# Kernel tuning notes

Measured on AMD Instinct MI355X. Metric: run time of the kernel, lower is better.

Reference implementation:

```python
import jax, jax.numpy as jnp
import numpy as np
import math

DIM = 1024
NUM_HEADS = 16
HEAD_DIM = DIM // NUM_HEADS
WINDOW = 256


def setup_inputs() -> dict:
    key = jax.random.key(0)
    k1, k2, k3 = jax.random.split(key, 3)
    B, T = 2, 2048
    x = jax.random.normal(k1, (B, T, DIM), dtype=jnp.float32)
    # nn.Linear weights: [out, in]; y = x @ W.T
    w_qkv = jax.random.normal(k2, (3 * DIM, DIM), dtype=jnp.float32) * (1.0 / math.sqrt(DIM))
    w_out = jax.random.normal(k3, (DIM, DIM), dtype=jnp.float32) * (1.0 / math.sqrt(DIM))
    return {"x": x, "w_qkv": w_qkv, "w_out": w_out}


def _apply_rotary(x, cos, sin):
    # x: [B,H,T,D]; cos/sin: [T, D//2] broadcast over B,H
    d = x.shape[-1] // 2
    x1, x2 = x[..., :d], x[..., d:]
    return jnp.concatenate([x1 * cos - x2 * sin, x2 * cos + x1 * sin], axis=-1)


def reference(x, w_qkv, w_out):
    B, T, C = x.shape
    H, Dh = NUM_HEADS, HEAD_DIM
    qkv = (x @ w_qkv.T).reshape(B, T, 3, H, Dh)
    q, k, v = qkv[:, :, 0], qkv[:, :, 1], qkv[:, :, 2]  # [B,T,H,Dh]
    q = jnp.transpose(q, (0, 2, 1, 3))  # [B,H,T,Dh]
    k = jnp.transpose(k, (0, 2, 1, 3))
    v = jnp.transpose(v, (0, 2, 1, 3))
    # RoPE tables
    inv_freq = 1.0 / (10000.0 ** (jnp.arange(0, Dh, 2, dtype=jnp.float32) / Dh))
    t = jnp.arange(T, dtype=jnp.float32)
    freqs = jnp.einsum('i,j->ij', t, inv_freq)  # [T, Dh//2]
    cos, sin = jnp.cos(freqs), jnp.sin(freqs)
    q = _apply_rotary(q, cos, sin)
    k = _apply_rotary(k, cos, sin)
    scale = 1.0 / math.sqrt(Dh)
    attn = jnp.einsum('bhqd,bhkd->bhqk', q, k) * scale  # [B,H,T,T]
    i = jnp.arange(T)[:, None]
    j = jnp.arange(T)[None, :]
    allowed = (j <= i) & ((i - j) < WINDOW)  # causal + sliding window
    attn = jnp.where(allowed, attn, -jnp.inf)
    attn = jax.nn.softmax(attn, axis=-1)
    out = jnp.einsum('bhqk,bhkd->bhqd', attn, v)
    out = jnp.transpose(out, (0, 2, 1, 3)).reshape(B, T, C)
    return out @ w_out.T
```

## Files before the change

### kernel.cpp

```cpp
#include <hip/hip_runtime.h>
#include <stdint.h>
#include <math.h>

#define T_SEQ 2048
#define NHEAD 16
#define WIN 256

typedef unsigned short u16;
typedef __attribute__((ext_vector_type(8))) short short8;
typedef __attribute__((ext_vector_type(4))) float f32x4;

typedef const __attribute__((address_space(1))) void* gas_ptr;
typedef __attribute__((address_space(3))) void* las_ptr;

__device__ __forceinline__ u16 f2bf(float f) {
  uint32_t u = __builtin_bit_cast(uint32_t, f);
  u += 0x7fffu + ((u >> 16) & 1u);
  return (u16)(u >> 16);
}
__device__ __forceinline__ float bf2f(u16 v) {
  return __builtin_bit_cast(float, ((uint32_t)v) << 16);
}
__device__ __forceinline__ void g2l16(const u16* g, u16* l) {
  __builtin_amdgcn_global_load_lds((gas_ptr)g, (las_ptr)l, 16, 0, 0);
}

__global__ __launch_bounds__(256) void cast_bf16_k(const float* __restrict__ in,
                                                   u16* __restrict__ out, int n4) {
  int i = blockIdx.x * 256 + threadIdx.x;
  if (i >= n4) return;
  const float4 v = reinterpret_cast<const float4*>(in)[i];
  union { u16 h[4]; uint64_t q; } o;
  o.h[0] = f2bf(v.x); o.h[1] = f2bf(v.y); o.h[2] = f2bf(v.z); o.h[3] = f2bf(v.w);
  reinterpret_cast<uint64_t*>(out)[i] = o.q;
}

template <typename OUT_T>
__global__ __launch_bounds__(256) void gemm_nt(const u16* __restrict__ A,
                                               const u16* __restrict__ B,
                                               OUT_T* __restrict__ C,
                                               int M, int N, int K) {
  __shared__ u16 lA[128 * 32];
  __shared__ u16 lB[128 * 32];
  const int tid = threadIdx.x;
  const int lane = tid & 63;
  const int wave = tid >> 6;
  const int bm = blockIdx.y, bn = blockIdx.x;
  const int r = lane & 15, g = lane >> 4;
  const int wr = wave >> 1, wc = wave & 1;

  const u16* Abase = A + (size_t)bm * 128 * K;
  const u16* Bbase = B + (size_t)bn * 128 * K;

  f32x4 acc[4][4];
#pragma unroll
  for (int m = 0; m < 4; m++)
#pragma unroll
    for (int n = 0; n < 4; n++) acc[m][n] = (f32x4){0.f, 0.f, 0.f, 0.f};

  const int row0 = tid >> 2, kc0 = (tid & 3) * 8;
  const int row1 = (256 + tid) >> 2, kc1 = ((256 + tid) & 3) * 8;
  u16* lA0 = lA + (size_t)(wave * 64) * 8;
  u16* lA1 = lA + (size_t)(256 + wave * 64) * 8;
  u16* lB0 = lB + (size_t)(wave * 64) * 8;
  u16* lB1 = lB + (size_t)(256 + wave * 64) * 8;

  for (int k0 = 0; k0 < K; k0 += 32) {
    g2l16(Abase + (size_t)row0 * K + k0 + kc0, lA0);
    g2l16(Abase + (size_t)row1 * K + k0 + kc1, lA1);
    g2l16(Bbase + (size_t)row0 * K + k0 + kc0, lB0);
    g2l16(Bbase + (size_t)row1 * K + k0 + kc1, lB1);
    __syncthreads();
    short8 af[4], bfr[4];
#pragma unroll
    for (int m = 0; m < 4; m++)
      af[m] = *reinterpret_cast<const short8*>(&lA[(wr * 64 + m * 16 + r) * 32 + g * 8]);
#pragma unroll
    for (int n = 0; n < 4; n++)
      bfr[n] = *reinterpret_cast<const short8*>(&lB[(wc * 64 + n * 16 + r) * 32 + g * 8]);
#pragma unroll
    for (int m = 0; m < 4; m++)
#pragma unroll
      for (int n = 0; n < 4; n++)
        acc[m][n] = __builtin_amdgcn_mfma_f32_16x16x32_bf16(af[m], bfr[n], acc[m][n], 0, 0, 0);
    __syncthreads();
  }

#pragma unroll
  for (int m = 0; m < 4; m++) {
    const int row = bm * 128 + wr * 64 + m * 16 + g * 4;
#pragma unroll
    for (int n = 0; n < 4; n++) {
      const int col = bn * 128 + wc * 64 + n * 16 + r;
#pragma unroll
      for (int j = 0; j < 4; j++) {
        float v = acc[m][n][j];
        if constexpr (sizeof(OUT_T) == 2)
          C[(size_t)(row + j) * N + col] = f2bf(v);
        else
          C[(size_t)(row + j) * N + col] = v;
      }
    }
  }
}

__global__ __launch_bounds__(256) void rope_qk(const u16* __restrict__ qkv,
                                               u16* __restrict__ Qb,
                                               u16* __restrict__ Kb) {
  int idx = blockIdx.x * 256 + threadIdx.x;
  int d = idx & 31;
  int t = (idx >> 5) & (T_SEQ - 1);
  int h = (idx >> 16) & (NHEAD - 1);
  int b = idx >> 20;
  size_t mrow = ((size_t)(b * T_SEQ + t)) * 3072;
  int hd = h * 64 + d;
  float q1 = bf2f(qkv[mrow + hd]);
  float q2 = bf2f(qkv[mrow + hd + 32]);
  float k1 = bf2f(qkv[mrow + 1024 + hd]);
  float k2 = bf2f(qkv[mrow + 1024 + hd + 32]);
  float inv = exp2f(-(float)d * 0.41524101186092029f);
  float ang = (float)t * inv;
  float s, c;
  __sincosf(ang, &s, &c);
  size_t orow = ((size_t)((b * NHEAD + h) * T_SEQ + t)) * 64 + d;
  Qb[orow]      = f2bf(q1 * c - q2 * s);
  Qb[orow + 32] = f2bf(q2 * c + q1 * s);
  Kb[orow]      = f2bf(k1 * c - k2 * s);
  Kb[orow + 32] = f2bf(k2 * c + k1 * s);
}

__global__ __launch_bounds__(256) void v_trans(const u16* __restrict__ qkv,
                                               u16* __restrict__ Vt) {
  __shared__ u16 tile[64][72];
  const int t0 = blockIdx.x * 64;
  const int bh = blockIdx.y;
  const int b = bh >> 4, h = bh & 15;
  const int tid = threadIdx.x;
#pragma unroll
  for (int it = 0; it < 16; it++) {
    int idx = it * 256 + tid;
    int tl = idx >> 6, d = idx & 63;
    tile[tl][d] = qkv[((size_t)(b * T_SEQ + t0 + tl)) * 3072 + 2048 + h * 64 + d];
  }
  __syncthreads();
#pragma unroll
  for (int it = 0; it < 16; it++) {
    int idx = it * 256 + tid;
    int d = idx >> 6, tl = idx & 63;
    Vt[((size_t)bh * 64 + d) * T_SEQ + t0 + tl] = tile[tl][d];
  }
}

__device__ __forceinline__ void stage_kv(const u16* __restrict__ Kh,
                                         const u16* __restrict__ Vh, int k0,
                                         u16* lk, u16* lv, int tid) {
  const int wave = tid >> 6;
#pragma unroll
  for (int p = 0; p < 2; p++) {
    int c = p * 256 + tid;
    int row = c >> 3;
    int col = ((c & 7) ^ (row & 7)) * 8;
    g2l16(Kh + (size_t)(k0 + row) * 64 + col, lk + p * 2048 + wave * 512);
    g2l16(Vh + (size_t)row * T_SEQ + k0 + col, lv + p * 2048 + wave * 512);
  }
}

__global__ __launch_bounds__(256) void attn_k(const u16* __restrict__ Qb,
                                              const u16* __restrict__ Kb,
                                              const u16* __restrict__ Vt,
                                              u16* __restrict__ Ob) {
  const int bid = blockIdx.x;
  const int owned = (bid & 7) * 128 + (bid >> 3);
  const int qt = owned & 31;
  const int bh = owned >> 5;

  const int tid = threadIdx.x, lane = tid & 63, w = tid >> 6;
  const int r = lane & 15, g = lane >> 4;
  const int q0 = qt * 64;
  const u16* Qh = Qb + (size_t)bh * T_SEQ * 64;
  const u16* Kh = Kb + (size_t)bh * T_SEQ * 64;
  const u16* Vh = Vt + (size_t)bh * 64 * T_SEQ;

  __shared__ u16 lK[2][64 * 64];
  __shared__ u16 lV[2][64 * 64];
  __shared__ u16 p_lds[4][16][72];

  short8 aq[2];
#pragma unroll
  for (int kk = 0; kk < 2; kk++)
    aq[kk] = *reinterpret_cast<const short8*>(
        &Qh[(size_t)(q0 + w * 16 + r) * 64 + kk * 32 + g * 8]);

  f32x4 o[4];
#pragma unroll
  for (int n = 0; n < 4; n++) o[n] = (f32x4){0.f, 0.f, 0.f, 0.f};
  float mrun[4], lrun[4];
#pragma unroll
  for (int j = 0; j < 4; j++) { mrun[j] = -1e30f; lrun[j] = 0.f; }

  const int ktlo = (qt >= 4) ? (qt - 4) : 0;
  stage_kv(Kh, Vh, qt * 64, lK[0], lV[0], tid);
  __syncthreads();
  int buf = 0;

  for (int kt = qt; kt >= ktlo; kt--) {
    const int k0 = kt * 64;
    if (kt > ktlo)
      stage_kv(Kh, Vh, (kt - 1) * 64, lK[buf ^ 1], lV[buf ^ 1], tid);

    const u16* lk = lK[buf];
    const u16* lv = lV[buf];
    const int sw = (r & 7) * 8;

    f32x4 s[4];
#pragma unroll
    for (int n = 0; n < 4; n++) {
      f32x4 sn = (f32x4){0.f, 0.f, 0.f, 0.f};
#pragma unroll
      for (int kk = 0; kk < 2; kk++) {
        short8 bk = *reinterpret_cast<const short8*>(
            &lk[(n * 16 + r) * 64 + ((kk * 32 + g * 8) ^ sw)]);
        sn = __builtin_amdgcn_mfma_f32_16x16x32_bf16(aq[kk], bk, sn, 0, 0, 0);
      }
      s[n] = sn;
    }
    float rmax[4] = {-1e30f, -1e30f, -1e30f, -1e30f};
#pragma unroll
    for (int n = 0; n < 4; n++) {
      const int k = k0 + n * 16 + r;
#pragma unroll
      for (int j = 0; j < 4; j++) {
        const int q = q0 + w * 16 + g * 4 + j;
        float v = s[n][j] * 0.125f;
        bool ok = (k <= q) && (q - k < WIN);
        v = ok ? v : -1e30f;
        s[n][j] = v;
        rmax[j] = fmaxf(rmax[j], v);
      }
    }
#pragma unroll
    for (int off = 1; off < 16; off <<= 1)
#pragma unroll
      for (int j = 0; j < 4; j++) rmax[j] = fmaxf(rmax[j], __shfl_xor(rmax[j], off));

    float scl[4];
#pragma unroll
    for (int j = 0; j < 4; j++) {
      float mn = fmaxf(mrun[j], rmax[j]);
      scl[j] = __expf(mrun[j] - mn);
      mrun[j] = mn;
    }
    float rsum[4] = {0.f, 0.f, 0.f, 0.f};
#pragma unroll
    for (int n = 0; n < 4; n++)
#pragma unroll
      for (int j = 0; j < 4; j++) {
        float p = __expf(s[n][j] - mrun[j]);
        s[n][j] = p;
        rsum[j] += p;
      }
#pragma unroll
    for (int off = 1; off < 16; off <<= 1)
#pragma unroll
      for (int j = 0; j < 4; j++) rsum[j] += __shfl_xor(rsum[j], off);
#pragma unroll
    for (int j = 0; j < 4; j++) lrun[j] = lrun[j] * scl[j] + rsum[j];
#pragma unroll
    for (int n = 0; n < 4; n++)
#pragma unroll
      for (int j = 0; j < 4; j++) o[n][j] *= scl[j];

#pragma unroll
    for (int n = 0; n < 4; n++)
#pragma unroll
      for (int j = 0; j < 4; j++) p_lds[w][g * 4 + j][n * 16 + r] = f2bf(s[n][j]);
#pragma unroll
    for (int kk = 0; kk < 2; kk++) {
      short8 ap = *reinterpret_cast<const short8*>(&p_lds[w][r][kk * 32 + g * 8]);
#pragma unroll
      for (int n = 0; n < 4; n++) {
        short8 bv = *reinterpret_cast<const short8*>(
            &lv[(n * 16 + r) * 64 + ((kk * 32 + g * 8) ^ sw)]);
        o[n] = __builtin_amdgcn_mfma_f32_16x16x32_bf16(ap, bv, o[n], 0, 0, 0);
      }
    }
    __syncthreads();
    buf ^= 1;
  }

  const int b = bh >> 4, h = bh & 15;
#pragma unroll
  for (int n = 0; n < 4; n++)
#pragma unroll
    for (int j = 0; j < 4; j++) {
      const int q = q0 + w * 16 + g * 4 + j;
      size_t off = ((size_t)(b * T_SEQ + q)) * 1024 + h * 64 + n * 16 + r;
      Ob[off] = f2bf(o[n][j] / lrun[j]);
    }
}

extern "C" void kernel_launch(void* const* d_in, const int* in_sizes, int n_in,
                              void* d_out, int out_size, void* d_ws, size_t ws_size,
                              hipStream_t stream) {
  const float* x = (const float*)d_in[0];
  const float* w_qkv = (const float*)d_in[1];
  const float* w_out = (const float*)d_in[2];
  float* out = (float*)d_out;
  char* ws = (char*)d_ws;

  u16* xb    = (u16*)(ws + 0);
  u16* wqkvb = (u16*)(ws + 8388608);
  u16* qkvb  = (u16*)(ws + 16777216);
  u16* Qb    = (u16*)(ws + 0);
  u16* Kb    = (u16*)(ws + 8388608);
  u16* Vt    = (u16*)(ws + 41943040);
  u16* woutb = (u16*)(ws + 50331648);
  u16* Ob    = (u16*)(ws + 16777216);

  cast_bf16_k<<<4096, 256, 0, stream>>>(x, xb, 1048576);
  cast_bf16_k<<<3072, 256, 0, stream>>>(w_qkv, wqkvb, 786432);
  cast_bf16_k<<<1024, 256, 0, stream>>>(w_out, woutb, 262144);

  gemm_nt<u16><<<dim3(24, 32), 256, 0, stream>>>(xb, wqkvb, qkvb, 4096, 3072, 1024);

  rope_qk<<<8192, 256, 0, stream>>>(qkvb, Qb, Kb);
  v_trans<<<dim3(32, 32), 256, 0, stream>>>(qkvb, Vt);

  attn_k<<<1024, 256, 0, stream>>>(Qb, Kb, Vt, Ob);

  gemm_nt<float><<<dim3(8, 32), 256, 0, stream>>>(Ob, woutb, out, 4096, 1024, 1024);
}
```

Before: 185.4 us.

## Double-buffer GEMM LDS tiles, swizzle LDS layout, and remap blocks per XCD

The GEMM now keeps two LDS buffers so the async global-to-LDS load of the next K-slice is issued before the MFMAs on the current one, with one barrier per iteration instead of two. The LDS layout XOR-swizzles the 8-element column chunks by row to reduce bank conflicts on the short8 fragment reads. Launch changes to a 1D grid, and block IDs are remapped so each XCD (bid & 7) gets a contiguous set of N-column tiles, aiming for better L2 reuse of B. The cost is double the LDS footprint, which may reduce occupancy.

```diff
diff --git a/kernel.cpp b/kernel.cpp
--- a/kernel.cpp
+++ b/kernel.cpp
@@ -40,15 +40,21 @@
                                                const u16* __restrict__ B,
                                                OUT_T* __restrict__ C,
                                                int M, int N, int K) {
-  __shared__ u16 lA[128 * 32];
-  __shared__ u16 lB[128 * 32];
+  __shared__ u16 lA[2][128 * 32];
+  __shared__ u16 lB[2][128 * 32];
   const int tid = threadIdx.x;
   const int lane = tid & 63;
   const int wave = tid >> 6;
-  const int bm = blockIdx.y, bn = blockIdx.x;
   const int r = lane & 15, g = lane >> 4;
   const int wr = wave >> 1, wc = wave & 1;
 
+  const int nbn = N >> 7;
+  const int bnpx = nbn >> 3;
+  const int bid = blockIdx.x;
+  const int xcd = bid & 7, ii = bid >> 3;
+  const int bn = xcd * bnpx + (ii % bnpx);
+  const int bm = ii / bnpx;
+
   const u16* Abase = A + (size_t)bm * 128 * K;
   const u16* Bbase = B + (size_t)bn * 128 * K;
 
@@ -58,32 +64,44 @@
 #pragma unroll
     for (int n = 0; n < 4; n++) acc[m][n] = (f32x4){0.f, 0.f, 0.f, 0.f};
 
-  const int row0 = tid >> 2, kc0 = (tid & 3) * 8;
-  const int row1 = (256 + tid) >> 2, kc1 = ((256 + tid) & 3) * 8;
-  u16* lA0 = lA + (size_t)(wave * 64) * 8;
-  u16* lA1 = lA + (size_t)(256 + wave * 64) * 8;
-  u16* lB0 = lB + (size_t)(wave * 64) * 8;
-  u16* lB1 = lB + (size_t)(256 + wave * 64) * 8;
-
+  const int c0 = tid, c1 = 256 + tid;
+  const int row0 = c0 >> 2, row1 = c1 >> 2;
+  const int sw0 = ((c0 & 3) ^ (row0 & 3)) * 8;
+  const int sw1 = ((c1 & 3) ^ (row1 & 3)) * 8;
+  const int ldsb = wave * 512;
+
+  auto stage = [&](int k0, int b) {
+    g2l16(Abase + (size_t)row0 * K + k0 + sw0, &lA[b][ldsb]);
+    g2l16(Abase + (size_t)row1 * K + k0 + sw1, &lA[b][2048 + ldsb]);
+    g2l16(Bbase + (size_t)row0 * K + k0 + sw0, &lB[b][ldsb]);
+    g2l16(Bbase + (size_t)row1 * K + k0 + sw1, &lB[b][2048 + ldsb]);
+  };
+
+  stage(0, 0);
+  __syncthreads();
+  int buf = 0;
+
+  const int rsw = (r & 3);
   for (int k0 = 0; k0 < K; k0 += 32) {
-    g2l16(Abase + (size_t)row0 * K + k0 + kc0, lA0);
-    g2l16(Abase + (size_t)row1 * K + k0 + kc1, lA1);
-    g2l16(Bbase + (size_t)row0 * K + k0 + kc0, lB0);
-    g2l16(Bbase + (size_t)row1 * K + k0 + kc1, lB1);
-    __syncthreads();
+    if (k0 + 32 < K) stage(k0 + 32, buf ^ 1);
+    const u16* la = lA[buf];
+    const u16* lb = lB[buf];
     short8 af[4], bfr[4];
 #pragma unroll
     for (int m = 0; m < 4; m++)
-      af[m] = *reinterpret_cast<const short8*>(&lA[(wr * 64 + m * 16 + r) * 32 + g * 8]);
+      af[m] = *reinterpret_cast<const short8*>(
+          &la[(wr * 64 + m * 16 + r) * 32 + ((g ^ rsw) * 8)]);
 #pragma unroll
     for (int n = 0; n < 4; n++)
-      bfr[n] = *reinterpret_cast<const short8*>(&lB[(wc * 64 + n * 16 + r) * 32 + g * 8]);
+      bfr[n] = *reinterpret_cast<const short8*>(
+          &lb[(wc * 64 + n * 16 + r) * 32 + ((g ^ rsw) * 8)]);
 #pragma unroll
     for (int m = 0; m < 4; m++)
 #pragma unroll
       for (int n = 0; n < 4; n++)
         acc[m][n] = __builtin_amdgcn_mfma_f32_16x16x32_bf16(af[m], bfr[n], acc[m][n], 0, 0, 0);
     __syncthreads();
+    buf ^= 1;
   }
 
 #pragma unroll
@@ -321,12 +339,12 @@
   cast_bf16_k<<<3072, 256, 0, stream>>>(w_qkv, wqkvb, 786432);
   cast_bf16_k<<<1024, 256, 0, stream>>>(w_out, woutb, 262144);
 
-  gemm_nt<u16><<<dim3(24, 32), 256, 0, stream>>>(xb, wqkvb, qkvb, 4096, 3072, 1024);
+  gemm_nt<u16><<<768, 256, 0, stream>>>(xb, wqkvb, qkvb, 4096, 3072, 1024);
 
   rope_qk<<<8192, 256, 0, stream>>>(qkvb, Qb, Kb);
   v_trans<<<dim3(32, 32), 256, 0, stream>>>(qkvb, Vt);
 
   attn_k<<<1024, 256, 0, stream>>>(Qb, Kb, Vt, Ob);
 
-  gemm_nt<float><<<dim3(8, 32), 256, 0, stream>>>(Ob, woutb, out, 4096, 1024, 1024);
-}
+  gemm_nt<float><<<256, 256, 0, stream>>>(Ob, woutb, out, 4096, 1024, 1024);
+}
```

Result: faster. 181.0 us (-2.4%).
